# Performance work log

Measured on AMD Instinct MI355X. Metric: run time of the kernel, lower is better.

The kernel has to match this reference:

```python
import jax, jax.numpy as jnp
import numpy as np

H = 128           # hidden_size
N_NODE = 100000   # item vocab
B = 1024          # sessions
NODES_PER = 50
N = B * NODES_PER # total session nodes
E = 8 * N         # edges


def setup_inputs() -> dict:
    key = jax.random.key(0)
    ks = jax.random.split(key, 16)
    stdv = 1.0 / np.sqrt(H)
    u = lambda k, shape: jax.random.uniform(k, shape, jnp.float32, -stdv, stdv)
    x = jax.random.randint(ks[0], (N,), 1, N_NODE + 1)      # 1-indexed items
    edge_index = jax.random.randint(ks[1], (2, E), 0, N)
    batch = jnp.repeat(jnp.arange(B), NODES_PER)            # sorted segment ids
    return {
        "x": x, "edge_index": edge_index, "batch": batch,
        "emb_weight": u(ks[2], (N_NODE, H)),
        "W_gconv": u(ks[3], (H, H)),
        "W_ih": u(ks[4], (3 * H, H)), "W_hh": u(ks[5], (3 * H, H)),
        "b_ih": u(ks[6], (3 * H,)), "b_hh": u(ks[7], (3 * H,)),
        "W1_w": u(ks[8], (H, H)), "W1_b": u(ks[9], (H,)),
        "W2_w": u(ks[10], (H, H)), "W2_b": u(ks[11], (H,)),
        "q_w": u(ks[12], (1, H)), "q_b": u(ks[13], (1,)),
        "W3_w": u(ks[14], (H, 2 * H)), "W3_b": u(ks[15], (H,)),
    }


def _forward(x, edge_index, batch, emb_weight, W_gconv, W_ih, W_hh, b_ih, b_hh,
             W1_w, W1_b, W2_w, W2_b, q_w, q_b, W3_w, W3_b):
    n = x.shape[0]
    h = emb_weight[x - 1]                                   # [N, H]
    # GatedGraphConv, num_layers=1: linear -> scatter-add -> GRUCell
    m = h @ W_gconv                                          # [N, H]
    agg = jax.ops.segment_sum(m[edge_index[0]], edge_index[1], num_segments=n)
    gi = agg @ W_ih.T + b_ih                                 # [N, 3H]
    gh = h @ W_hh.T + b_hh
    i_r, i_z, i_n = jnp.split(gi, 3, axis=1)
    h_r, h_z, h_n = jnp.split(gh, 3, axis=1)
    r = jax.nn.sigmoid(i_r + h_r)
    z = jax.nn.sigmoid(i_z + h_z)
    ng = jnp.tanh(i_n + r * h_n)
    h = (1.0 - z) * ng + z * h
    h = jax.nn.relu(h)
    # Embedding2Score: segment-wise attention readout
    last_idx = jax.ops.segment_max(jnp.arange(n), batch, num_segments=B)
    v_n = h[last_idx]                                        # [B, H] last node per session
    a = jax.nn.sigmoid(v_n[batch] @ W1_w.T + W1_b + h @ W2_w.T + W2_b)
    alpha = a @ q_w.T + q_b                                  # [N, 1]
    s_g = jax.ops.segment_sum(alpha * h, batch, num_segments=B)  # [B, H]
    s_h = jnp.concatenate([v_n, s_g], axis=1) @ W3_w.T + W3_b    # [B, H]
    return s_h @ emb_weight.T                                # [B, n_node]


def reference(x, edge_index, batch, emb_weight, W_gconv, W_ih, W_hh, b_ih, b_hh,
              W1_w, W1_b, W2_w, W2_b, q_w, q_b, W3_w, W3_b):
    return _forward(x, edge_index, batch, emb_weight, W_gconv, W_ih, W_hh, b_ih, b_hh,
                    W1_w, W1_b, W2_w, W2_b, q_w, q_b, W3_w, W3_b)
```

## Files before the change

### kernel.cpp

```cpp
#include <hip/hip_runtime.h>
#include <math.h>

#define NNODES 51200
#define NEDGES 409600
#define NB 1024
#define NODES_PER 50
#define NVOCAB 100000
#define NVPAD 100096
#define SLOTS 64

typedef __attribute__((ext_vector_type(8))) short bf16x8;
typedef __attribute__((ext_vector_type(4))) float f32x4;

__device__ __forceinline__ float sigf(float x) { return 1.0f / (1.0f + __expf(-x)); }

__device__ __forceinline__ ushort f2bf(float x) {
    union { float f; unsigned u; } v; v.f = x;
    const unsigned r = v.u + 0x7FFF + ((v.u >> 16) & 1);
    return (ushort)(r >> 16);
}
__device__ __forceinline__ float bf2f(ushort u) {
    union { float f; unsigned u; } v; v.u = ((unsigned)u) << 16; return v.f;
}
__device__ __forceinline__ bf16x8 cvt8(const float* __restrict__ src) {
    const float4 v0 = *(const float4*)src, v1 = *(const float4*)(src + 4);
    bf16x8 p;
    p[0] = (short)f2bf(v0.x); p[1] = (short)f2bf(v0.y);
    p[2] = (short)f2bf(v0.z); p[3] = (short)f2bf(v0.w);
    p[4] = (short)f2bf(v1.x); p[5] = (short)f2bf(v1.y);
    p[6] = (short)f2bf(v1.z); p[7] = (short)f2bf(v1.w);
    return p;
}

__global__ __launch_bounds__(256)
void gemm_bf16(ushort* __restrict__ Cout, const float* __restrict__ A,
               const float* __restrict__ B) {
    __shared__ float4 smemv[4096];
    ushort* As = (ushort*)smemv;
    ushort* Bs = As + 128 * 128;
    const int m0 = blockIdx.x * 128;
    const int t  = threadIdx.x;

    #pragma unroll
    for (int f = t; f < 2048; f += 256) {
        const int r = f >> 4, c8 = (f & 15) * 8;
        *(bf16x8*)&As[r * 128 + (c8 ^ ((r & 7) << 3))] = cvt8(A + (size_t)(m0 + r) * 128 + c8);
        *(bf16x8*)&Bs[r * 128 + (c8 ^ ((r & 7) << 3))] = cvt8(B + (size_t)r * 128 + c8);
    }
    __syncthreads();

    const int lane = t & 63, wid = t >> 6;
    const int wr = wid >> 1, wc = wid & 1;
    const int l15 = lane & 15, kg = (lane >> 4) * 8;

    f32x4 acc[4][4] = {};
    #pragma unroll
    for (int kc = 0; kc < 4; ++kc) {
        const int cs = kc * 32 + kg;
        bf16x8 af[4], bfr[4];
        #pragma unroll
        for (int i = 0; i < 4; ++i) {
            const int ra = wr * 64 + i * 16 + l15;
            af[i] = *(const bf16x8*)&As[ra * 128 + (cs ^ ((ra & 7) << 3))];
            const int rb = wc * 64 + i * 16 + l15;
            bfr[i] = *(const bf16x8*)&Bs[rb * 128 + (cs ^ ((rb & 7) << 3))];
        }
        #pragma unroll
        for (int i = 0; i < 4; ++i)
            #pragma unroll
            for (int j = 0; j < 4; ++j)
                acc[i][j] = __builtin_amdgcn_mfma_f32_16x16x32_bf16(af[i], bfr[j], acc[i][j], 0, 0, 0);
    }
    const int cr0 = (lane >> 4) * 4;
    #pragma unroll
    for (int j = 0; j < 4; ++j) {
        const int col = wc * 64 + j * 16 + l15;
        #pragma unroll
        for (int i = 0; i < 4; ++i) {
            const int row = m0 + wr * 64 + i * 16 + cr0;
            #pragma unroll
            for (int q = 0; q < 4; ++q)
                Cout[(size_t)(row + q) * 128 + col] = f2bf(acc[i][j][q]);
        }
    }
}

__global__ __launch_bounds__(256)
void prep_kernel(const int* __restrict__ x, const float* __restrict__ emb,
                 ushort* __restrict__ hb, const int* __restrict__ ei,
                 int* __restrict__ cnt, int* __restrict__ esrc,
                 ushort* __restrict__ embswz) {
    const int bid = blockIdx.x;
    const int t = threadIdx.x;
    if (bid < 3200) {
        const int tid = bid * 256 + t;
        const int i = tid >> 4, c8 = (tid & 15) * 8;
        const int idx = x[i] - 1;
        *(bf16x8*)(hb + (size_t)i * 128 + c8) = cvt8(emb + (size_t)idx * 128 + c8);
    } else if (bid < 4800) {
        const int e = (bid - 3200) * 256 + t;
        const int dst = ei[NEDGES + e];
        const int pos = atomicAdd(&cnt[dst], 1);
        if (pos < SLOTS) esrc[(size_t)dst * SLOTS + pos] = ei[e];
    } else {
        const int f = (bid - 4800) * 256 + t;
        const int row = f >> 4, c8 = (f & 15) * 8;
        bf16x8 pk = {0, 0, 0, 0, 0, 0, 0, 0};
        if (row < NVOCAB) pk = cvt8(emb + (size_t)row * 128 + c8);
        *(bf16x8*)&embswz[(size_t)row * 128 + (c8 ^ ((row & 7) << 3))] = pk;
    }
}

__global__ __launch_bounds__(256)
void agg_kernel(const int* __restrict__ cnt, const int* __restrict__ esrc,
                const ushort* __restrict__ hb, ushort* __restrict__ aggb) {
    const int node = blockIdx.x * 4 + (threadIdx.x >> 6);
    const int l = threadIdx.x & 63;
    int cn = cnt[node]; if (cn > SLOTS) cn = SLOTS;
    const int* es = esrc + (size_t)node * SLOTS;
    float ax = 0.f, ay = 0.f;
    for (int j = 0; j < cn; ++j) {
        const int src = es[j];
        const unsigned u = *(const unsigned*)(hb + (size_t)src * 128 + l * 2);
        ax += bf2f((ushort)(u & 0xffff));
        ay += bf2f((ushort)(u >> 16));
    }
    const unsigned o = (unsigned)f2bf(ax) | ((unsigned)f2bf(ay) << 16);
    *(unsigned*)(aggb + (size_t)node * 128 + l * 2) = o;
}

__global__ __launch_bounds__(512)
void gru_fused(const ushort* __restrict__ aggb, const ushort* __restrict__ Wc,
               const float* __restrict__ Whh, const float* __restrict__ bih,
               const float* __restrict__ bhh, ushort* __restrict__ hb) {
    __shared__ ushort As[128 * 128];
    __shared__ ushort Bs[384 * 128];
    const int m0 = blockIdx.x * 128;
    const int t = threadIdx.x;
    const int lane = t & 63, wid = t >> 6;
    const int l15 = lane & 15, kg = (lane >> 4) * 8;

    #pragma unroll
    for (int f = t; f < 2048; f += 512) {
        const int r = f >> 4, c8 = (f & 15) * 8;
        const bf16x8 pk = *(const bf16x8*)(aggb + (size_t)(m0 + r) * 128 + c8);
        *(bf16x8*)&As[r * 128 + (c8 ^ ((r & 7) << 3))] = pk;
    }
    #pragma unroll
    for (int f = t; f < 6144; f += 512) {
        const int r = f >> 4, c8 = (f & 15) * 8;
        const bf16x8 pk = *(const bf16x8*)(Wc + (size_t)r * 128 + c8);
        *(bf16x8*)&Bs[r * 128 + (c8 ^ ((r & 7) << 3))] = pk;
    }
    __syncthreads();

    f32x4 gi[24] = {};
    #pragma unroll
    for (int kc = 0; kc < 4; ++kc) {
        const int cs = kc * 32 + kg;
        const int ra = wid * 16 + l15;
        const bf16x8 af = *(const bf16x8*)&As[ra * 128 + (cs ^ ((ra & 7) << 3))];
        #pragma unroll
        for (int j = 0; j < 24; ++j) {
            const int rb = j * 16 + l15;
            const bf16x8 bfr = *(const bf16x8*)&Bs[rb * 128 + (cs ^ ((rb & 7) << 3))];
            gi[j] = __builtin_amdgcn_mfma_f32_16x16x32_bf16(af, bfr, gi[j], 0, 0, 0);
        }
    }
    __syncthreads();

    #pragma unroll
    for (int f = t; f < 2048; f += 512) {
        const int r = f >> 4, c8 = (f & 15) * 8;
        const bf16x8 pk = *(const bf16x8*)(hb + (size_t)(m0 + r) * 128 + c8);
        *(bf16x8*)&As[r * 128 + (c8 ^ ((r & 7) << 3))] = pk;
    }
    #pragma unroll
    for (int f = t; f < 6144; f += 512) {
        const int r = f >> 4, c8 = (f & 15) * 8;
        *(bf16x8*)&Bs[r * 128 + (c8 ^ ((r & 7) << 3))] = cvt8(Whh + (size_t)r * 128 + c8);
    }
    __syncthreads();

    f32x4 gh[24] = {};
    #pragma unroll
    for (int kc = 0; kc < 4; ++kc) {
        const int cs = kc * 32 + kg;
        const int ra = wid * 16 + l15;
        const bf16x8 af = *(const bf16x8*)&As[ra * 128 + (cs ^ ((ra & 7) << 3))];
        #pragma unroll
        for (int j = 0; j < 24; ++j) {
            const int rb = j * 16 + l15;
            const bf16x8 bfr = *(const bf16x8*)&Bs[rb * 128 + (cs ^ ((rb & 7) << 3))];
            gh[j] = __builtin_amdgcn_mfma_f32_16x16x32_bf16(af, bfr, gh[j], 0, 0, 0);
        }
    }

    const int lr0 = wid * 16 + (lane >> 4) * 4;
    #pragma unroll
    for (int j = 0; j < 8; ++j) {
        const int col = j * 16 + l15;
        const float bir = bih[col], biz = bih[128 + col], bin = bih[256 + col];
        const float bhr = bhh[col], bhz = bhh[128 + col], bhn = bhh[256 + col];
        #pragma unroll
        for (int q = 0; q < 4; ++q) {
            const int lr = lr0 + q;
            const int adr = lr * 128 + (col ^ ((lr & 7) << 3));
            const float hv = bf2f(As[adr]);
            const float r_ = sigf(gi[j][q] + bir + gh[j][q] + bhr);
            const float z  = sigf(gi[j + 8][q] + biz + gh[j + 8][q] + bhz);
            const float ng = tanhf(gi[j + 16][q] + bin + r_ * (gh[j + 16][q] + bhn));
            As[adr] = f2bf(fmaxf((1.f - z) * ng + z * hv, 0.f));
        }
    }
    __syncthreads();
    #pragma unroll
    for (int f = t; f < 2048; f += 512) {
        const int r = f >> 4, c8 = (f & 15) * 8;
        *(bf16x8*)(hb + (size_t)(m0 + r) * 128 + c8) =
            *(const bf16x8*)&As[r * 128 + (c8 ^ ((r & 7) << 3))];
    }
}

__global__ __launch_bounds__(256)
void attn_sh(const ushort* __restrict__ hb, const float* __restrict__ W1,
             const float* __restrict__ b1, const float* __restrict__ W2,
             const float* __restrict__ qw, const float* __restrict__ qbp,
             const float* __restrict__ b2, const float* __restrict__ W3,
             const float* __restrict__ b3, float* __restrict__ sh) {
    __shared__ ushort As[128 * 128];
    __shared__ ushort Bs[128 * 128];
    __shared__ float t1s[2][128];
    __shared__ float qws[128];
    __shared__ float apar[2][2][64];
    __shared__ float alph[2][64];
    __shared__ float sgs[2][128];
    const int m0 = blockIdx.x * 100;
    const int t = threadIdx.x;
    const int lane = t & 63, wid = t >> 6;
    const int wr = wid >> 1, wc = wid & 1;
    const int l15 = lane & 15, kg = (lane >> 4) * 8;
    const int cr0 = (lane >> 4) * 4;

    #pragma unroll
    for (int f = t; f < 2048; f += 256) {
        const int r = f >> 4, c8 = (f & 15) * 8;
        int gr = m0 + r; if (gr > NNODES - 1) gr = NNODES - 1;
        *(bf16x8*)&As[r * 128 + (c8 ^ ((r & 7) << 3))] =
            *(const bf16x8*)(hb + (size_t)gr * 128 + c8);
        *(bf16x8*)&Bs[r * 128 + (c8 ^ ((r & 7) << 3))] = cvt8(W2 + (size_t)r * 128 + c8);
    }
    if (t < 128) qws[t] = qw[t];
    __syncthreads();

    f32x4 acc[4][4] = {};
    #pragma unroll
    for (int kc = 0; kc < 4; ++kc) {
        const int cs = kc * 32 + kg;
        bf16x8 af[4], bfr[4];
        #pragma unroll
        for (int i = 0; i < 4; ++i) {
            const int ra = wr * 64 + i * 16 + l15;
            af[i] = *(const bf16x8*)&As[ra * 128 + (cs ^ ((ra & 7) << 3))];
            const int rb = wc * 64 + i * 16 + l15;
            bfr[i] = *(const bf16x8*)&Bs[rb * 128 + (cs ^ ((rb & 7) << 3))];
        }
        #pragma unroll
        for (int i = 0; i < 4; ++i)
            #pragma unroll
            for (int j = 0; j < 4; ++j)
                acc[i][j] = __builtin_amdgcn_mfma_f32_16x16x32_bf16(af[i], bfr[j], acc[i][j], 0, 0, 0);
    }
    __syncthreads();

    #pragma unroll
    for (int j = 0; j < 4; ++j) {
        const int col = wc * 64 + j * 16 + l15;
        const int csw = (col & 7) << 3;
        #pragma unroll
        for (int i = 0; i < 4; ++i) {
            const int row = wr * 64 + i * 16 + cr0;
            #pragma unroll
            for (int q = 0; q < 4; ++q)
                Bs[col * 128 + ((row + q) ^ csw)] = f2bf(acc[i][j][q]);
        }
    }

    const int sess = wid >> 1, half = wid & 1;
    const int d = half * 64 + lane;
    const int vrow = sess * 50 + 49;
    const int vsw = (vrow & 7) << 3;
    float t1v = b1[d] + b2[d];
    const float* w1r = W1 + (size_t)d * 128;
    #pragma unroll 8
    for (int k = 0; k < 128; k += 4) {
        const float4 w = *(const float4*)(w1r + k);
        t1v += w.x * bf2f(As[vrow * 128 + ((k + 0) ^ vsw)])
             + w.y * bf2f(As[vrow * 128 + ((k + 1) ^ vsw)])
             + w.z * bf2f(As[vrow * 128 + ((k + 2) ^ vsw)])
             + w.w * bf2f(As[vrow * 128 + ((k + 3) ^ vsw)]);
    }
    t1s[sess][d] = t1v;
    __syncthreads();

    float p = 0.f;
    if (lane < 50) {
        const int row = sess * 50 + lane;
        const int d0 = half * 64;
        #pragma unroll 8
        for (int dd = d0; dd < d0 + 64; ++dd)
            p += qws[dd] * sigf(t1s[sess][dd] + bf2f(Bs[dd * 128 + (row ^ ((dd & 7) << 3))]));
    }
    apar[sess][half][lane] = p;
    __syncthreads();
    if (half == 0 && lane < 50)
        alph[sess][lane] = apar[sess][0][lane] + apar[sess][1][lane] + qbp[0];
    __syncthreads();

    float sacc = 0.f;
    #pragma unroll 10
    for (int i = 0; i < 50; ++i) {
        const int row = sess * 50 + i;
        sacc += alph[sess][i] * bf2f(As[row * 128 + (d ^ ((row & 7) << 3))]);
    }
    sgs[sess][d] = sacc;
    __syncthreads();

    float shacc = b3[d];
    const float* w3r = W3 + (size_t)d * 256;
    #pragma unroll 8
    for (int k = 0; k < 128; k += 4) {
        const float4 w = *(const float4*)(w3r + k);
        shacc += w.x * bf2f(As[vrow * 128 + ((k + 0) ^ vsw)])
               + w.y * bf2f(As[vrow * 128 + ((k + 1) ^ vsw)])
               + w.z * bf2f(As[vrow * 128 + ((k + 2) ^ vsw)])
               + w.w * bf2f(As[vrow * 128 + ((k + 3) ^ vsw)]);
    }
    #pragma unroll 8
    for (int k = 0; k < 128; k += 4) {
        const float4 w = *(const float4*)(w3r + 128 + k);
        shacc += w.x * sgs[sess][k] + w.y * sgs[sess][k + 1]
               + w.z * sgs[sess][k + 2] + w.w * sgs[sess][k + 3];
    }
    sh[(size_t)(blockIdx.x * 2 + sess) * 128 + d] = shacc;
}

__global__ __launch_bounds__(256)
void gemm_vocab(float* __restrict__ C, const float* __restrict__ A,
                const ushort* __restrict__ Bswz) {
    __shared__ ushort As[128 * 128];
    __shared__ ushort Bs[128 * 128];
    float* Cs = (float*)Bs;
    const int id = blockIdx.x;
    const int xcd = id & 7, loc = id >> 3;
    const int mt = loc & 7, gin = loc >> 3;
    const int grp = xcd * 25 + gin;
    const int m0 = mt * 128;
    const int t = threadIdx.x;
    const int lane = t & 63, wid = t >> 6;
    const int wr = wid >> 1, wc = wid & 1;
    const int l15 = lane & 15, kg = (lane >> 4) * 8;
    const int cr0 = (lane >> 4) * 4;

    #pragma unroll
    for (int f = t; f < 2048; f += 256) {
        const int r = f >> 4, c8 = (f & 15) * 8;
        *(bf16x8*)&As[r * 128 + (c8 ^ ((r & 7) << 3))] = cvt8(A + (size_t)(m0 + r) * 128 + c8);
    }

    for (int it = 0; it < 4; ++it) {
        const int n0 = (grp * 4 + it) * 128;
        if (n0 >= NVOCAB) break;
        __syncthreads();
        const ushort* srcb = Bswz + (size_t)n0 * 128;
        #pragma unroll
        for (int f = t; f < 2048; f += 256)
            *(bf16x8*)&Bs[f * 8] = *(const bf16x8*)(srcb + f * 8);
        __syncthreads();

        f32x4 acc[4][4] = {};
        #pragma unroll
        for (int kc = 0; kc < 4; ++kc) {
            const int cs = kc * 32 + kg;
            bf16x8 af[4], bfr[4];
            #pragma unroll
            for (int i = 0; i < 4; ++i) {
                const int ra = wr * 64 + i * 16 + l15;
                af[i] = *(const bf16x8*)&As[ra * 128 + (cs ^ ((ra & 7) << 3))];
                const int rb = wc * 64 + i * 16 + l15;
                bfr[i] = *(const bf16x8*)&Bs[rb * 128 + (cs ^ ((rb & 7) << 3))];
            }
            #pragma unroll
            for (int i = 0; i < 4; ++i)
                #pragma unroll
                for (int j = 0; j < 4; ++j)
                    acc[i][j] = __builtin_amdgcn_mfma_f32_16x16x32_bf16(af[i], bfr[j], acc[i][j], 0, 0, 0);
        }
        __syncthreads();

        #pragma unroll
        for (int half = 0; half < 2; ++half) {
            if (wr == half) {
                #pragma unroll
                for (int j = 0; j < 4; ++j) {
                    const int col = wc * 64 + j * 16 + l15;
                    #pragma unroll
                    for (int i = 0; i < 4; ++i) {
                        const int rl = i * 16 + cr0;
                        #pragma unroll
                        for (int q = 0; q < 4; ++q)
                            Cs[(rl + q) * 128 + col] = acc[i][j][q];
                    }
                }
            }
            __syncthreads();
            #pragma unroll
            for (int f = t; f < 2048; f += 256) {
                const int r = f >> 5, c4 = (f & 31) * 4;
                if (n0 + c4 < NVOCAB) {
                    const f32x4 v = *(const f32x4*)&Cs[r * 128 + c4];
                    *(f32x4*)(C + (size_t)(m0 + half * 64 + r) * NVOCAB + n0 + c4) = v;
                }
            }
            __syncthreads();
        }
    }
}

extern "C" void kernel_launch(void* const* d_in, const int* in_sizes, int n_in,
                              void* d_out, int out_size, void* d_ws, size_t ws_size,
                              hipStream_t stream) {
    const int*   x   = (const int*)d_in[0];
    const int*   ei  = (const int*)d_in[1];
    const float* emb = (const float*)d_in[3];
    const float* Wg  = (const float*)d_in[4];
    const float* Wih = (const float*)d_in[5];
    const float* Whh = (const float*)d_in[6];
    const float* bih = (const float*)d_in[7];
    const float* bhh = (const float*)d_in[8];
    const float* W1  = (const float*)d_in[9];
    const float* b1  = (const float*)d_in[10];
    const float* W2  = (const float*)d_in[11];
    const float* b2  = (const float*)d_in[12];
    const float* qw  = (const float*)d_in[13];
    const float* qb  = (const float*)d_in[14];
    const float* W3  = (const float*)d_in[15];
    const float* b3  = (const float*)d_in[16];
    float* out = (float*)d_out;

    float*  ws     = (float*)d_ws;
    ushort* hb     = (ushort*)ws;
    ushort* aggb   = (ushort*)(ws + 3276800);
    ushort* Wc     = (ushort*)(ws + 6553600);
    float*  sh     = ws + 6578176;
    ushort* embswz = (ushort*)(ws + 6709248);
    int*    cnt    = (int*)(ws + 13115392);
    int*    esrc   = cnt + NNODES;

    hipMemsetAsync(cnt, 0, NNODES * sizeof(int), stream);

    gemm_bf16<<<3, 256, 0, stream>>>(Wc, Wih, Wg);
    prep_kernel<<<4800 + NVPAD / 16, 256, 0, stream>>>(x, emb, hb, ei, cnt, esrc, embswz);

    agg_kernel<<<12800, 256, 0, stream>>>(cnt, esrc, hb, aggb);

    gru_fused<<<400, 512, 0, stream>>>(aggb, Wc, Whh, bih, bhh, hb);

    attn_sh<<<512, 256, 0, stream>>>(hb, W1, b1, W2, qw, qb, b2, W3, b3, sh);

    gemm_vocab<<<1600, 256, 0, stream>>>(out, sh, embswz);
}
```

Baseline: 317.4 us.

## Fold weight-combine into prep kernel and restructure vocab GEMM with prefetch

```diff
diff --git a/kernel.cpp b/kernel.cpp
--- a/kernel.cpp
+++ b/kernel.cpp
@@ -33,63 +33,11 @@
 }
 
 __global__ __launch_bounds__(256)
-void gemm_bf16(ushort* __restrict__ Cout, const float* __restrict__ A,
-               const float* __restrict__ B) {
-    __shared__ float4 smemv[4096];
-    ushort* As = (ushort*)smemv;
-    ushort* Bs = As + 128 * 128;
-    const int m0 = blockIdx.x * 128;
-    const int t  = threadIdx.x;
-
-    #pragma unroll
-    for (int f = t; f < 2048; f += 256) {
-        const int r = f >> 4, c8 = (f & 15) * 8;
-        *(bf16x8*)&As[r * 128 + (c8 ^ ((r & 7) << 3))] = cvt8(A + (size_t)(m0 + r) * 128 + c8);
-        *(bf16x8*)&Bs[r * 128 + (c8 ^ ((r & 7) << 3))] = cvt8(B + (size_t)r * 128 + c8);
-    }
-    __syncthreads();
-
-    const int lane = t & 63, wid = t >> 6;
-    const int wr = wid >> 1, wc = wid & 1;
-    const int l15 = lane & 15, kg = (lane >> 4) * 8;
-
-    f32x4 acc[4][4] = {};
-    #pragma unroll
-    for (int kc = 0; kc < 4; ++kc) {
-        const int cs = kc * 32 + kg;
-        bf16x8 af[4], bfr[4];
-        #pragma unroll
-        for (int i = 0; i < 4; ++i) {
-            const int ra = wr * 64 + i * 16 + l15;
-            af[i] = *(const bf16x8*)&As[ra * 128 + (cs ^ ((ra & 7) << 3))];
-            const int rb = wc * 64 + i * 16 + l15;
-            bfr[i] = *(const bf16x8*)&Bs[rb * 128 + (cs ^ ((rb & 7) << 3))];
-        }
-        #pragma unroll
-        for (int i = 0; i < 4; ++i)
-            #pragma unroll
-            for (int j = 0; j < 4; ++j)
-                acc[i][j] = __builtin_amdgcn_mfma_f32_16x16x32_bf16(af[i], bfr[j], acc[i][j], 0, 0, 0);
-    }
-    const int cr0 = (lane >> 4) * 4;
-    #pragma unroll
-    for (int j = 0; j < 4; ++j) {
-        const int col = wc * 64 + j * 16 + l15;
-        #pragma unroll
-        for (int i = 0; i < 4; ++i) {
-            const int row = m0 + wr * 64 + i * 16 + cr0;
-            #pragma unroll
-            for (int q = 0; q < 4; ++q)
-                Cout[(size_t)(row + q) * 128 + col] = f2bf(acc[i][j][q]);
-        }
-    }
-}
-
-__global__ __launch_bounds__(256)
 void prep_kernel(const int* __restrict__ x, const float* __restrict__ emb,
                  ushort* __restrict__ hb, const int* __restrict__ ei,
                  int* __restrict__ cnt, int* __restrict__ esrc,
-                 ushort* __restrict__ embswz) {
+                 ushort* __restrict__ embswz, const float* __restrict__ Wih,
+                 const float* __restrict__ Wg, ushort* __restrict__ Wc) {
     const int bid = blockIdx.x;
     const int t = threadIdx.x;
     if (bid < 3200) {
@@ -102,12 +50,22 @@
         const int dst = ei[NEDGES + e];
         const int pos = atomicAdd(&cnt[dst], 1);
         if (pos < SLOTS) esrc[(size_t)dst * SLOTS + pos] = ei[e];
-    } else {
+    } else if (bid < 11056) {
         const int f = (bid - 4800) * 256 + t;
         const int row = f >> 4, c8 = (f & 15) * 8;
         bf16x8 pk = {0, 0, 0, 0, 0, 0, 0, 0};
         if (row < NVOCAB) pk = cvt8(emb + (size_t)row * 128 + c8);
         *(bf16x8*)&embswz[(size_t)row * 128 + (c8 ^ ((row & 7) << 3))] = pk;
+    } else {
+        const int idx = (bid - 11056) * 256 + t;
+        const int mrow = idx >> 7, n = idx & 127;
+        const float* wr = Wih + (size_t)mrow * 128;
+        const float* gr = Wg + (size_t)n * 128;
+        float acc = 0.f;
+        #pragma unroll 8
+        for (int k = 0; k < 128; ++k)
+            acc = fmaf(wr[k], gr[k], acc);
+        Wc[idx] = f2bf(acc);
     }
 }
 
@@ -227,7 +185,7 @@
              const float* __restrict__ b1, const float* __restrict__ W2,
              const float* __restrict__ qw, const float* __restrict__ qbp,
              const float* __restrict__ b2, const float* __restrict__ W3,
-             const float* __restrict__ b3, float* __restrict__ sh) {
+             const float* __restrict__ b3, ushort* __restrict__ shb) {
     __shared__ ushort As[128 * 128];
     __shared__ ushort Bs[128 * 128];
     __shared__ float t1s[2][128];
@@ -342,87 +300,92 @@
         shacc += w.x * sgs[sess][k] + w.y * sgs[sess][k + 1]
                + w.z * sgs[sess][k + 2] + w.w * sgs[sess][k + 3];
     }
-    sh[(size_t)(blockIdx.x * 2 + sess) * 128 + d] = shacc;
-}
-
-__global__ __launch_bounds__(256)
-void gemm_vocab(float* __restrict__ C, const float* __restrict__ A,
+    const int orow = blockIdx.x * 2 + sess;
+    shb[(size_t)orow * 128 + (d ^ ((orow & 7) << 3))] = f2bf(shacc);
+}
+
+__global__ __launch_bounds__(512)
+void gemm_vocab(float* __restrict__ C, const ushort* __restrict__ Ab,
                 const ushort* __restrict__ Bswz) {
     __shared__ ushort As[128 * 128];
     __shared__ ushort Bs[128 * 128];
-    float* Cs = (float*)Bs;
+    __shared__ float Cs[128 * 132];
     const int id = blockIdx.x;
     const int xcd = id & 7, loc = id >> 3;
     const int mt = loc & 7, gin = loc >> 3;
     const int grp = xcd * 25 + gin;
     const int m0 = mt * 128;
+    const int start = grp * 4;
+    int nt = 782 - start; if (nt > 4) nt = 4;
+    if (nt <= 0) return;
     const int t = threadIdx.x;
     const int lane = t & 63, wid = t >> 6;
-    const int wr = wid >> 1, wc = wid & 1;
+    const int wm = wid >> 2, wn = wid & 3;
     const int l15 = lane & 15, kg = (lane >> 4) * 8;
     const int cr0 = (lane >> 4) * 4;
 
     #pragma unroll
-    for (int f = t; f < 2048; f += 256) {
-        const int r = f >> 4, c8 = (f & 15) * 8;
-        *(bf16x8*)&As[r * 128 + (c8 ^ ((r & 7) << 3))] = cvt8(A + (size_t)(m0 + r) * 128 + c8);
-    }
-
-    for (int it = 0; it < 4; ++it) {
-        const int n0 = (grp * 4 + it) * 128;
-        if (n0 >= NVOCAB) break;
-        __syncthreads();
-        const ushort* srcb = Bswz + (size_t)n0 * 128;
-        #pragma unroll
-        for (int f = t; f < 2048; f += 256)
+    for (int f = t; f < 2048; f += 512)
+        *(bf16x8*)&As[f * 8] = *(const bf16x8*)(Ab + (size_t)m0 * 128 + f * 8);
+    {
+        const ushort* srcb = Bswz + (size_t)start * 128 * 128;
+        #pragma unroll
+        for (int f = t; f < 2048; f += 512)
             *(bf16x8*)&Bs[f * 8] = *(const bf16x8*)(srcb + f * 8);
-        __syncthreads();
-
-        f32x4 acc[4][4] = {};
+    }
+    __syncthreads();
+
+    for (int it = 0; it < nt; ++it) {
+        const int n0 = (start + it) * 128;
+        f32x4 acc[4][2] = {};
         #pragma unroll
         for (int kc = 0; kc < 4; ++kc) {
             const int cs = kc * 32 + kg;
-            bf16x8 af[4], bfr[4];
+            bf16x8 af[4], bfr[2];
             #pragma unroll
             for (int i = 0; i < 4; ++i) {
-                const int ra = wr * 64 + i * 16 + l15;
+                const int ra = wm * 64 + i * 16 + l15;
                 af[i] = *(const bf16x8*)&As[ra * 128 + (cs ^ ((ra & 7) << 3))];
-                const int rb = wc * 64 + i * 16 + l15;
-                bfr[i] = *(const bf16x8*)&Bs[rb * 128 + (cs ^ ((rb & 7) << 3))];
+            }
+            #pragma unroll
+            for (int j = 0; j < 2; ++j) {
+                const int rb = wn * 32 + j * 16 + l15;
+                bfr[j] = *(const bf16x8*)&Bs[rb * 128 + (cs ^ ((rb & 7) << 3))];
             }
             #pragma unroll
             for (int i = 0; i < 4; ++i)
                 #pragma unroll
-                for (int j = 0; j < 4; ++j)
+                for (int j = 0; j < 2; ++j)
                     acc[i][j] = __builtin_amdgcn_mfma_f32_16x16x32_bf16(af[i], bfr[j], acc[i][j], 0, 0, 0);
         }
         __syncthreads();
 
         #pragma unroll
-        for (int half = 0; half < 2; ++half) {
-            if (wr == half) {
+        for (int j = 0; j < 2; ++j) {
+            const int col = wn * 32 + j * 16 + l15;
+            #pragma unroll
+            for (int i = 0; i < 4; ++i) {
+                const int row = wm * 64 + i * 16 + cr0;
                 #pragma unroll
-                for (int j = 0; j < 4; ++j) {
-                    const int col = wc * 64 + j * 16 + l15;
-                    #pragma unroll
-                    for (int i = 0; i < 4; ++i) {
-                        const int rl = i * 16 + cr0;
-                        #pragma unroll
-                        for (int q = 0; q < 4; ++q)
-                            Cs[(rl + q) * 128 + col] = acc[i][j][q];
-                    }
-                }
+                for (int q = 0; q < 4; ++q)
+                    Cs[(row + q) * 132 + col] = acc[i][j][q];
             }
-            __syncthreads();
-            #pragma unroll
-            for (int f = t; f < 2048; f += 256) {
-                const int r = f >> 5, c4 = (f & 31) * 4;
-                if (n0 + c4 < NVOCAB) {
-                    const f32x4 v = *(const f32x4*)&Cs[r * 128 + c4];
-                    *(f32x4*)(C + (size_t)(m0 + half * 64 + r) * NVOCAB + n0 + c4) = v;
-                }
+        }
+        if (it + 1 < nt) {
+            const ushort* srcb = Bswz + (size_t)(n0 + 128) * 128;
+            #pragma unroll
+            for (int f = t; f < 2048; f += 512)
+                *(bf16x8*)&Bs[f * 8] = *(const bf16x8*)(srcb + f * 8);
+        }
+        __syncthreads();
+
+        #pragma unroll
+        for (int f = t; f < 4096; f += 512) {
+            const int r = f >> 5, c4 = (f & 31) * 4;
+            if (n0 + c4 < NVOCAB) {
+                const f32x4 v = *(const f32x4*)&Cs[r * 132 + c4];
+                *(f32x4*)(C + (size_t)(m0 + r) * NVOCAB + n0 + c4) = v;
             }
-            __syncthreads();
         }
     }
 }
@@ -452,21 +415,21 @@
     ushort* hb     = (ushort*)ws;
     ushort* aggb   = (ushort*)(ws + 3276800);
     ushort* Wc     = (ushort*)(ws + 6553600);
-    float*  sh     = ws + 6578176;
-    ushort* embswz = (ushort*)(ws + 6709248);
-    int*    cnt    = (int*)(ws + 13115392);
+    ushort* shb    = (ushort*)(ws + 6578176);
+    ushort* embswz = (ushort*)(ws + 6643712);
+    int*    cnt    = (int*)(ws + 13049856);
     int*    esrc   = cnt + NNODES;
 
     hipMemsetAsync(cnt, 0, NNODES * sizeof(int), stream);
 
-    gemm_bf16<<<3, 256, 0, stream>>>(Wc, Wih, Wg);
-    prep_kernel<<<4800 + NVPAD / 16, 256, 0, stream>>>(x, emb, hb, ei, cnt, esrc, embswz);
+    prep_kernel<<<11248, 256, 0, stream>>>(x, emb, hb, ei, cnt, esrc, embswz,
+                                           Wih, Wg, Wc);
 
     agg_kernel<<<12800, 256, 0, stream>>>(cnt, esrc, hb, aggb);
 
     gru_fused<<<400, 512, 0, stream>>>(aggb, Wc, Whh, bih, bhh, hb);
 
-    attn_sh<<<512, 256, 0, stream>>>(hb, W1, b1, W2, qw, qb, b2, W3, b3, sh);
-
-    gemm_vocab<<<1600, 256, 0, stream>>>(out, sh, embswz);
-}
+    attn_sh<<<512, 256, 0, stream>>>(hb, W1, b1, W2, qw, qb, b2, W3, b3, shb);
+
+    gemm_vocab<<<1600, 512, 0, stream>>>(out, shb, embswz);
+}
```

Result: no change. 323.0 us (+1.8%).
